# Performance work log

Measured on AMD Instinct MI355X. Metric: run time of the kernel, lower is better.

## Reference

```python
import jax, jax.numpy as jnp
import numpy as np
from functools import partial

NUM_HEADS = 8
EPS = 1e-12  # torch F.normalize default eps


def conv1x1(x, w):
    # x: [b,i,h,w], w: [o,i] -> [b,o,h,w]
    return jnp.einsum('oi,bihw->bohw', w, x)


def dwconv3x3(x, w):
    # depthwise 3x3, SAME padding; x: [b,c,h,w], w: [c,1,3,3]
    c = x.shape[1]
    return jax.lax.conv_general_dilated(
        x, w, window_strides=(1, 1), padding='SAME',
        dimension_numbers=('NCHW', 'OIHW', 'NCHW'), feature_group_count=c)


def setup_inputs() -> dict:
    key = jax.random.key(0)
    ks = jax.random.split(key, 16)
    b, dim, h, w = 2, 128, 256, 256
    d8 = dim // 8
    f = lambda k, shape, fan: (jax.random.normal(k, shape, jnp.float32) * (1.0 / np.sqrt(fan)))
    return {
        'x': jax.random.normal(ks[0], (b, dim, h, w), jnp.float32),
        'y': jax.random.normal(ks[1], (b, dim, h, w), jnp.float32),
        'qkv_w': f(ks[2], (dim * 3, dim), dim),
        'qkv_dw_w': f(ks[3], (dim * 3, 1, 3, 3), 9),
        'proj_w': f(ks[4], (dim, dim), dim),
        'sa_w1': f(ks[5], (d8, dim), dim),
        'sa_w2': f(ks[6], (d8, d8), d8),
        'sa_w3': f(ks[7], (1, d8), d8),
        'sp_w1': f(ks[8], (d8, dim), dim),
        'sp_w2': f(ks[9], (d8, d8), d8),
        'sp_w3': f(ks[10], (dim, d8), d8),
        'dw_w': f(ks[11], (dim, 1, 3, 3), 9),
        'temperature': jnp.ones((NUM_HEADS, 1, 1), jnp.float32),
    }


def reference(x, y, qkv_w, qkv_dw_w, proj_w, sa_w1, sa_w2, sa_w3,
              sp_w1, sp_w2, sp_w3, dw_w, temperature):
    b, c, h, w = x.shape
    hd = NUM_HEADS
    # QKV: 1x1 conv then depthwise 3x3
    qkv = dwconv3x3(conv1x1(x, qkv_w), qkv_dw_w)
    q, k, v = jnp.split(qkv, 3, axis=1)
    # Spatial attention gate from y: [b,1,h,w]
    sa = jax.nn.sigmoid(conv1x1(jax.nn.relu(conv1x1(jax.nn.relu(conv1x1(y, sa_w1)), sa_w2)), sa_w3))
    q = q * sa
    # b (head c) h w -> b head c (h w)
    shp = (b, hd, c // hd, h * w)
    q = q.reshape(shp)
    k = k.reshape(shp)
    v = v.reshape(shp)
    # L2 normalize along spatial axis (torch F.normalize semantics)
    q = q / jnp.maximum(jnp.linalg.norm(q, axis=-1, keepdims=True), EPS)
    k = k / jnp.maximum(jnp.linalg.norm(k, axis=-1, keepdims=True), EPS)
    # channel-wise attention: [b,head,c/head,c/head]
    attn = jnp.einsum('bhcn,bhdn->bhcd', q, k) * temperature
    attn = jax.nn.softmax(attn, axis=-1)
    out = jnp.einsum('bhcd,bhdn->bhcn', attn, v).reshape(b, c, h, w)
    # Spectral attention gate from out: [b,c]
    pooled = jnp.mean(out, axis=(2, 3))
    g = jax.nn.gelu(pooled @ sp_w1.T, approximate=False)
    g = jax.nn.gelu(g @ sp_w2.T, approximate=False)
    spec = jax.nn.sigmoid(g @ sp_w3.T)[:, :, None, None]
    y2 = dwconv3x3(y, dw_w) * spec
    return conv1x1(out + y2, proj_w)
```

## Files before the change

### kernel.cpp

```cpp
#include <hip/hip_runtime.h>
#include <hip/hip_bf16.h>

typedef __hip_bfloat16 bf16;
typedef __attribute__((ext_vector_type(8))) short short8;
typedef __attribute__((ext_vector_type(4))) int   int4v;
typedef __attribute__((ext_vector_type(4))) float float4v;

#define B_   2
#define C_   128
#define H_   256
#define W_   256
#define HW_  65536
#define HD_  8
#define CH_  16
#define C3_  384

static __device__ __forceinline__ float b2f(bf16 v) { return __bfloat162float(v); }
static __device__ __forceinline__ bf16  f2b(float v) { return __float2bfloat16(v); }
static __device__ __forceinline__ short b2s(bf16 v) { return *reinterpret_cast<short*>(&v); }
static __device__ __forceinline__ float su2f(short s) {
  return __uint_as_float(((unsigned)(unsigned short)s) << 16);
}
static __device__ __forceinline__ short8 smask(short8 v, int m) {
  int4v iv = *(int4v*)&v;
  iv = iv & m;
  return *(short8*)&iv;
}

__global__ void k_wprep(const float* __restrict__ qkv_w, const float* __restrict__ proj_w,
                        const float* __restrict__ sa_w1,
                        float* __restrict__ wt_qkvT, float* __restrict__ wt_proj,
                        float* __restrict__ wt_sa1, bf16* __restrict__ wt_qkv_bf,
                        bf16* __restrict__ wt_proj_bf, int do_bf) {
  int idx = blockIdx.x * 256 + threadIdx.x;
  if (idx < C3_ * C_) { int o = idx / C_, i = idx % C_; wt_qkvT[i * C3_ + o] = qkv_w[idx]; }
  if (idx < C_ * C_)  { int o = idx / C_, i = idx % C_; wt_proj[i * C_ + o] = proj_w[idx]; }
  if (idx < 16 * C_)  { int j = idx / C_, i = idx % C_; wt_sa1[i * 16 + j] = sa_w1[idx]; }
  if (do_bf && idx < C3_ * C_) {
    int o = idx / C_, k = idx % C_;
    int sk = ((((k >> 3) ^ (o & 7)) << 3) | (k & 7));
    wt_qkv_bf[o * C_ + sk] = f2b(qkv_w[idx]);
  }
  if (do_bf && idx < C_ * C_) {
    int o = idx / C_, k = idx % C_;
    int sk = ((((k >> 3) ^ (o & 7)) << 3) | (k & 7));
    wt_proj_bf[o * C_ + sk] = f2b(proj_w[idx]);
  }
}

__global__ void __launch_bounds__(256) k_sa(
    const float* __restrict__ y, const float* __restrict__ wt_sa1,
    const float* __restrict__ sa_w2, const float* __restrict__ sa_w3,
    float* __restrict__ sa) {
  int b = blockIdx.y;
  int p0 = (blockIdx.x * 256 + threadIdx.x) * 2;
  const float* yp = y + (size_t)b * C_ * HW_ + p0;
  float t1a[16], t1b[16];
#pragma unroll
  for (int j = 0; j < 16; ++j) { t1a[j] = 0.f; t1b[j] = 0.f; }
  for (int i = 0; i < C_; ++i) {
    float2 v = *(const float2*)(yp + (size_t)i * HW_);
    const float* wr = wt_sa1 + i * 16;
#pragma unroll
    for (int j = 0; j < 16; ++j) { t1a[j] = fmaf(wr[j], v.x, t1a[j]); t1b[j] = fmaf(wr[j], v.y, t1b[j]); }
  }
#pragma unroll
  for (int j = 0; j < 16; ++j) { t1a[j] = fmaxf(t1a[j], 0.f); t1b[j] = fmaxf(t1b[j], 0.f); }
  float t2a[16], t2b[16];
#pragma unroll
  for (int j = 0; j < 16; ++j) {
    float sx = 0.f, sy = 0.f;
#pragma unroll
    for (int l = 0; l < 16; ++l) { float w = sa_w2[j * 16 + l]; sx = fmaf(w, t1a[l], sx); sy = fmaf(w, t1b[l], sy); }
    t2a[j] = fmaxf(sx, 0.f); t2b[j] = fmaxf(sy, 0.f);
  }
  float sa3 = 0.f, sb3 = 0.f;
#pragma unroll
  for (int j = 0; j < 16; ++j) { float w = sa_w3[j]; sa3 = fmaf(w, t2a[j], sa3); sb3 = fmaf(w, t2b[j], sb3); }
  sa[(size_t)b * HW_ + p0]     = 1.f / (1.f + expf(-sa3));
  sa[(size_t)b * HW_ + p0 + 1] = 1.f / (1.f + expf(-sb3));
}

__global__ void __launch_bounds__(256) k_convm(
    const float* __restrict__ x, const bf16* __restrict__ wbf, bf16* __restrict__ pre) {
  __shared__ bf16 XT[2][64][128];
  __shared__ bf16 AT[128][128];
  int b = blockIdx.y;
  int p0 = blockIdx.x * 64;
  int t = threadIdx.x;

  {
    int p  = t & 63;
    int c0 = t >> 6;
    const float* xp = x + (size_t)b * C_ * HW_ + p0 + p;
#pragma unroll
    for (int it = 0; it < 4; ++it) {
      int c = c0 + it * 4;
      short8 hv, lv;
#pragma unroll
      for (int j = 0; j < 8; ++j) {
        float v = xp[(size_t)(c * 8 + j) * HW_];
        bf16 h = f2b(v);
        bf16 l = f2b(v - b2f(h));
        hv[j] = b2s(h); lv[j] = b2s(l);
      }
      int sc = c ^ (p & 7);
      *(short8*)&XT[0][p][sc * 8] = hv;
      *(short8*)&XT[1][p][sc * 8] = lv;
    }
  }

  int lane = t & 63, wave = t >> 6;
  int m = lane & 15, quad = lane >> 4;
  int wr = wave >> 1, wc = wave & 1;
  float4v acc[4][2];

  for (int mb = 0; mb < 3; ++mb) {
    __syncthreads();
    {
      const short8* src = (const short8*)(wbf + mb * C_ * C_);
      short8* dst = (short8*)&AT[0][0];
#pragma unroll
      for (int j = 0; j < 8; ++j)
        dst[j * 256 + t] = src[j * 256 + t];
    }
    __syncthreads();

#pragma unroll
    for (int mt = 0; mt < 4; ++mt)
#pragma unroll
      for (int nt = 0; nt < 2; ++nt)
#pragma unroll
        for (int e = 0; e < 4; ++e) acc[mt][nt][e] = 0.f;

#pragma unroll
    for (int kk = 0; kk < 4; ++kk) {
      int cidx = (((kk * 4 + quad) ^ (m & 7)) << 3);
      short8 af[4], bh[2], bl[2];
#pragma unroll
      for (int mt = 0; mt < 4; ++mt)
        af[mt] = *(const short8*)&AT[wr * 64 + mt * 16 + m][cidx];
#pragma unroll
      for (int nt = 0; nt < 2; ++nt) {
        bh[nt] = *(const short8*)&XT[0][wc * 32 + nt * 16 + m][cidx];
        bl[nt] = *(const short8*)&XT[1][wc * 32 + nt * 16 + m][cidx];
      }
#pragma unroll
      for (int mt = 0; mt < 4; ++mt)
#pragma unroll
        for (int nt = 0; nt < 2; ++nt) {
          acc[mt][nt] = __builtin_amdgcn_mfma_f32_16x16x32_bf16(af[mt], bh[nt], acc[mt][nt], 0, 0, 0);
          acc[mt][nt] = __builtin_amdgcn_mfma_f32_16x16x32_bf16(af[mt], bl[nt], acc[mt][nt], 0, 0, 0);
        }
    }

    bf16* op = pre + (size_t)b * C3_ * HW_ + (size_t)(mb * C_) * HW_ + p0;
#pragma unroll
    for (int mt = 0; mt < 4; ++mt)
#pragma unroll
      for (int nt = 0; nt < 2; ++nt)
#pragma unroll
        for (int reg = 0; reg < 4; ++reg) {
          int o = wr * 64 + mt * 16 + quad * 4 + reg;
          int p = wc * 32 + nt * 16 + m;
          op[(size_t)o * HW_ + p] = f2b(acc[mt][nt][reg]);
        }
  }
}

__global__ void __launch_bounds__(256) k_dwgram(
    const bf16* __restrict__ pre, const float* __restrict__ dww,
    const float* __restrict__ sa, float* __restrict__ attn_raw,
    float* __restrict__ ssq_q, float* __restrict__ ssq_k) {
  __shared__ char smem[65536];
  bf16 (*ring)[4][256][8] = (bf16 (*)[4][256][8])smem;
  bf16 (*dwb)[256] = (bf16 (*)[256])(smem + 49152);
  float* red = (float*)smem;

  int b = blockIdx.z, head = blockIdx.y, r0 = blockIdx.x * 8;
  int t = threadIdx.x;
  const bf16* preb = pre + (size_t)b * C3_ * HW_;
  const float* saw = sa + (size_t)b * HW_;

  auto loadrow = [&](int r) {
    int slot = (r + 3) % 3;
#pragma unroll
    for (int cg = 0; cg < 4; ++cg) {
      short8 hv;
      if (r < 0 || r >= H_) {
#pragma unroll
        for (int j = 0; j < 8; ++j) hv[j] = 0;
      } else {
#pragma unroll
        for (int j = 0; j < 8; ++j) {
          int c = cg * 8 + j;
          int och = (c < 16) ? (head * CH_ + c) : (C_ + head * CH_ + c - 16);
          hv[j] = b2s(preb[(size_t)och * HW_ + r * W_ + t]);
        }
      }
      *(short8*)&ring[slot][cg][t][0] = hv;
    }
  };
  loadrow(r0 - 1); loadrow(r0); loadrow(r0 + 1);
  __syncthreads();

  int lane = t & 63, wave = t >> 6;
  int m = lane & 15, quad = lane >> 4;
  int sch = t >> 3;
  int ccl = (t > 0) ? (t - 1) : 0;
  int ccr = (t < W_ - 1) ? (t + 1) : (W_ - 1);
  int mskl = (t > 0) ? -1 : 0;
  int mskr = (t < W_ - 1) ? -1 : 0;
  float4v acc = {0.f, 0.f, 0.f, 0.f};
  float sacc = 0.f;

  for (int rr = r0; rr < r0 + 8; ++rr) {
    float gate = saw[rr * W_ + t];
    float a[32];
#pragma unroll
    for (int c = 0; c < 32; ++c) a[c] = 0.f;
#pragma unroll
    for (int dy = -1; dy <= 1; ++dy) {
      int s = (rr + dy + 3) % 3;
#pragma unroll
      for (int cg = 0; cg < 4; ++cg) {
        const bf16* base = &ring[s][cg][0][0];
        short8 vl = smask(*(const short8*)(base + ccl * 8), mskl);
        short8 vc = *(const short8*)(base + (size_t)t * 8);
        short8 vr = smask(*(const short8*)(base + ccr * 8), mskr);
#pragma unroll
        for (int j = 0; j < 8; ++j) {
          int c = cg * 8 + j;
          int och = (c < 16) ? (head * CH_ + c) : (C_ + head * CH_ + c - 16);
          const float* wp = dww + och * 9 + (dy + 1) * 3;
          a[c] = fmaf(wp[0], su2f(vl[j]), a[c]);
          a[c] = fmaf(wp[1], su2f(vc[j]), a[c]);
          a[c] = fmaf(wp[2], su2f(vr[j]), a[c]);
        }
      }
    }
#pragma unroll
    for (int c = 0; c < 16; ++c) a[c] *= gate;
#pragma unroll
    for (int c = 0; c < 32; ++c) dwb[c][t ^ ((c & 7) << 3)] = f2b(a[c]);
    __syncthreads();
#pragma unroll
    for (int cn = 0; cn < 2; ++cn) {
      int p0 = wave * 64 + cn * 32;
      int ca = ((((p0 >> 3) + quad) ^ (m & 7)) << 3);
      short8 af = *(const short8*)&dwb[m][ca];
      short8 bfv = *(const short8*)&dwb[16 + m][ca];
      acc = __builtin_amdgcn_mfma_f32_16x16x32_bf16(af, bfv, acc, 0, 0, 0);
    }
#pragma unroll
    for (int it = 0; it < 4; ++it) {
      int c = (t & 7) + it * 8;
      int cs = c ^ (sch & 7);
      short8 v = *(const short8*)&dwb[sch][cs * 8];
#pragma unroll
      for (int j = 0; j < 8; ++j) { float f = su2f(v[j]); sacc = fmaf(f, f, sacc); }
    }
    if (rr < r0 + 7) loadrow(rr + 2);
    __syncthreads();
  }
  float* ar = attn_raw + ((size_t)b * HD_ + head) * 256;
#pragma unroll
  for (int reg = 0; reg < 4; ++reg)
    atomicAdd(&ar[(quad * 4 + reg) * 16 + m], acc[reg]);
  red[t] = sacc;
  __syncthreads();
  if (t < 32) {
    float s = 0.f;
#pragma unroll
    for (int k = 0; k < 8; ++k) s += red[t * 8 + k];
    if (t < 16) atomicAdd(&ssq_q[((size_t)b * HD_ + head) * CH_ + t], s);
    else        atomicAdd(&ssq_k[((size_t)b * HD_ + head) * CH_ + t - 16], s);
  }
}

__global__ void k_softmax(const float* __restrict__ attn_raw, const float* __restrict__ ssq_q,
                          const float* __restrict__ ssq_k, const float* __restrict__ temperature,
                          float* __restrict__ attn) {
  int row = threadIdx.x;
  int bh = row >> 4;
  int head = bh & 7;
  float temp = temperature[head];
  float nq = fmaxf(sqrtf(ssq_q[row]), 1e-12f);
  float v[16];
#pragma unroll
  for (int d = 0; d < 16; ++d) {
    float nk = fmaxf(sqrtf(ssq_k[bh * 16 + d]), 1e-12f);
    v[d] = attn_raw[row * 16 + d] / (nq * nk) * temp;
  }
  float m = -1e30f;
#pragma unroll
  for (int d = 0; d < 16; ++d) m = fmaxf(m, v[d]);
  float s = 0.f;
#pragma unroll
  for (int d = 0; d < 16; ++d) { v[d] = expf(v[d] - m); s += v[d]; }
  float inv = 1.f / s;
#pragma unroll
  for (int d = 0; d < 16; ++d) attn[row * 16 + d] = v[d] * inv;
}

__global__ void __launch_bounds__(256) k_out(
    const bf16* __restrict__ pre, const float* __restrict__ dww,
    const float* __restrict__ attn, float* __restrict__ outb) {
  __shared__ bf16 ring[3][2][256][8];
  int b = blockIdx.z, head = blockIdx.y, r0 = blockIdx.x * 8;
  int t = threadIdx.x;
  const bf16* preb = pre + (size_t)b * C3_ * HW_ + (size_t)(2 * C_ + head * CH_) * HW_;

  auto loadrow = [&](int r) {
    int slot = (r + 3) % 3;
#pragma unroll
    for (int cg = 0; cg < 2; ++cg) {
      short8 hv;
      if (r < 0 || r >= H_) {
#pragma unroll
        for (int j = 0; j < 8; ++j) hv[j] = 0;
      } else {
#pragma unroll
        for (int j = 0; j < 8; ++j)
          hv[j] = b2s(preb[(size_t)(cg * 8 + j) * HW_ + r * W_ + t]);
      }
      *(short8*)&ring[slot][cg][t][0] = hv;
    }
  };
  loadrow(r0 - 1); loadrow(r0); loadrow(r0 + 1);
  __syncthreads();
  const float* ap = attn + ((size_t)b * HD_ + head) * 256;
  int ccl = (t > 0) ? (t - 1) : 0;
  int ccr = (t < W_ - 1) ? (t + 1) : (W_ - 1);
  int mskl = (t > 0) ? -1 : 0;
  int mskr = (t < W_ - 1) ? -1 : 0;
  for (int rr = r0; rr < r0 + 8; ++rr) {
    float vv[16];
#pragma unroll
    for (int c = 0; c < 16; ++c) vv[c] = 0.f;
#pragma unroll
    for (int dy = -1; dy <= 1; ++dy) {
      int s = (rr + dy + 3) % 3;
#pragma unroll
      for (int cg = 0; cg < 2; ++cg) {
        const bf16* base = &ring[s][cg][0][0];
        short8 vl = smask(*(const short8*)(base + ccl * 8), mskl);
        short8 vc = *(const short8*)(base + (size_t)t * 8);
        short8 vr = smask(*(const short8*)(base + ccr * 8), mskr);
#pragma unroll
        for (int j = 0; j < 8; ++j) {
          int c = cg * 8 + j;
          const float* wp = dww + (2 * C_ + head * CH_ + c) * 9 + (dy + 1) * 3;
          vv[c] = fmaf(wp[0], su2f(vl[j]), vv[c]);
          vv[c] = fmaf(wp[1], su2f(vc[j]), vv[c]);
          vv[c] = fmaf(wp[2], su2f(vr[j]), vv[c]);
        }
      }
    }
    float* op = outb + ((size_t)b * C_ + head * CH_) * (size_t)HW_ + rr * W_ + t;
#pragma unroll
    for (int c2 = 0; c2 < 16; ++c2) {
      float s2 = 0.f;
#pragma unroll
      for (int d = 0; d < 16; ++d) s2 = fmaf(ap[c2 * 16 + d], vv[d], s2);
      op[(size_t)c2 * HW_] = s2;
    }
    __syncthreads();
    if (rr < r0 + 7) loadrow(rr + 2);
    __syncthreads();
  }
}

__global__ void k_pool(const float* __restrict__ outb, float* __restrict__ pooled) {
  int ch = blockIdx.x, b = blockIdx.y;
  const float* p = outb + ((size_t)b * C_ + ch) * (size_t)HW_;
  float s = 0.f;
  for (int i = threadIdx.x * 4; i < HW_; i += 1024) {
    float4 v = *(const float4*)(p + i);
    s += v.x + v.y + v.z + v.w;
  }
#pragma unroll
  for (int off = 32; off > 0; off >>= 1) s += __shfl_down(s, off);
  __shared__ float wsum[4];
  int lane = threadIdx.x & 63, wv = threadIdx.x >> 6;
  if (lane == 0) wsum[wv] = s;
  __syncthreads();
  if (threadIdx.x == 0) {
    float tt = wsum[0] + wsum[1] + wsum[2] + wsum[3];
    pooled[b * C_ + ch] = tt * (1.f / HW_);
  }
}

__global__ void k_spec(const float* __restrict__ pooled, const float* __restrict__ sp_w1,
                       const float* __restrict__ sp_w2, const float* __restrict__ sp_w3,
                       float* __restrict__ spec) {
  __shared__ float g1[2][16], g2[2][16];
  int tid = threadIdx.x;
  const float RS2 = 0.70710678118654752f;
  if (tid < 32) {
    int b = tid >> 4, j = tid & 15;
    float s = 0.f;
    for (int i = 0; i < C_; ++i) s = fmaf(sp_w1[j * C_ + i], pooled[b * C_ + i], s);
    g1[b][j] = 0.5f * s * (1.f + erff(s * RS2));
  }
  __syncthreads();
  if (tid < 32) {
    int b = tid >> 4, j = tid & 15;
    float s = 0.f;
    for (int l = 0; l < 16; ++l) s = fmaf(sp_w2[j * 16 + l], g1[b][l], s);
    g2[b][j] = 0.5f * s * (1.f + erff(s * RS2));
  }
  __syncthreads();
  {
    int b = tid >> 7, o = tid & 127;
    float s = 0.f;
    for (int jj = 0; jj < 16; ++jj) s = fmaf(sp_w3[o * 16 + jj], g2[b][jj], s);
    spec[b * C_ + o] = 1.f / (1.f + expf(-s));
  }
}

__global__ void __launch_bounds__(256) k_z(
    const float* __restrict__ y, const float* __restrict__ dww,
    const float* __restrict__ spec, float* __restrict__ dout) {
  int b = blockIdx.z, ch = blockIdx.y;
  int row = blockIdx.x * 4 + (threadIdx.x >> 6);
  int c0 = (threadIdx.x & 63) * 4;
  const float* yb = y + ((size_t)b * C_ + ch) * HW_;
  const float* wp = dww + ch * 9;
  float acc[4] = {0.f, 0.f, 0.f, 0.f};
#pragma unroll
  for (int dy = -1; dy <= 1; ++dy) {
    int rrow = row + dy;
    if (rrow < 0 || rrow >= H_) continue;
    const float* yr = yb + rrow * W_;
    float4 cv = *(const float4*)(yr + c0);
    float lf = (c0 > 0) ? yr[c0 - 1] : 0.f;
    float rt = (c0 + 4 < W_) ? yr[c0 + 4] : 0.f;
    float w0 = wp[(dy + 1) * 3], w1 = wp[(dy + 1) * 3 + 1], w2 = wp[(dy + 1) * 3 + 2];
    float v[6] = {lf, cv.x, cv.y, cv.z, cv.w, rt};
#pragma unroll
    for (int j = 0; j < 4; ++j)
      acc[j] = fmaf(w0, v[j], fmaf(w1, v[j + 1], fmaf(w2, v[j + 2], acc[j])));
  }
  float sp = spec[b * C_ + ch];
  float* dp = dout + ((size_t)b * C_ + ch) * HW_ + row * W_ + c0;
  float4 ov = *(const float4*)dp;
  ov.x += acc[0] * sp; ov.y += acc[1] * sp; ov.z += acc[2] * sp; ov.w += acc[3] * sp;
  *(float4*)dp = ov;
}

__global__ void __launch_bounds__(256) k_projm(
    const bf16* __restrict__ wpb, float* __restrict__ dout) {
  __shared__ bf16 XT[2][64][128];
  __shared__ bf16 AT[128][128];
  int b = blockIdx.y;
  int p0 = blockIdx.x * 64;
  int t = threadIdx.x;

  {
    const short8* src = (const short8*)wpb;
    short8* dst = (short8*)&AT[0][0];
#pragma unroll
    for (int j = 0; j < 8; ++j)
      dst[j * 256 + t] = src[j * 256 + t];
  }
  {
    int p  = t & 63;
    int c0 = t >> 6;
    const float* xp = dout + (size_t)b * C_ * HW_ + p0 + p;
#pragma unroll
    for (int it = 0; it < 4; ++it) {
      int c = c0 + it * 4;
      short8 hv, lv;
#pragma unroll
      for (int j = 0; j < 8; ++j) {
        float v = xp[(size_t)(c * 8 + j) * HW_];
        bf16 h = f2b(v);
        bf16 l = f2b(v - b2f(h));
        hv[j] = b2s(h); lv[j] = b2s(l);
      }
      int sc = c ^ (p & 7);
      *(short8*)&XT[0][p][sc * 8] = hv;
      *(short8*)&XT[1][p][sc * 8] = lv;
    }
  }
  __syncthreads();

  int lane = t & 63, wave = t >> 6;
  int m = lane & 15, quad = lane >> 4;
  int wr = wave >> 1, wc = wave & 1;
  float4v acc[4][2];
#pragma unroll
  for (int mt = 0; mt < 4; ++mt)
#pragma unroll
    for (int nt = 0; nt < 2; ++nt)
#pragma unroll
      for (int e = 0; e < 4; ++e) acc[mt][nt][e] = 0.f;

#pragma unroll
  for (int kk = 0; kk < 4; ++kk) {
    int cidx = (((kk * 4 + quad) ^ (m & 7)) << 3);
    short8 af[4], bh[2], bl[2];
#pragma unroll
    for (int mt = 0; mt < 4; ++mt)
      af[mt] = *(const short8*)&AT[wr * 64 + mt * 16 + m][cidx];
#pragma unroll
    for (int nt = 0; nt < 2; ++nt) {
      bh[nt] = *(const short8*)&XT[0][wc * 32 + nt * 16 + m][cidx];
      bl[nt] = *(const short8*)&XT[1][wc * 32 + nt * 16 + m][cidx];
    }
#pragma unroll
    for (int mt = 0; mt < 4; ++mt)
#pragma unroll
      for (int nt = 0; nt < 2; ++nt) {
        acc[mt][nt] = __builtin_amdgcn_mfma_f32_16x16x32_bf16(af[mt], bh[nt], acc[mt][nt], 0, 0, 0);
        acc[mt][nt] = __builtin_amdgcn_mfma_f32_16x16x32_bf16(af[mt], bl[nt], acc[mt][nt], 0, 0, 0);
      }
  }

  float* op = dout + (size_t)b * C_ * HW_ + p0;
#pragma unroll
  for (int mt = 0; mt < 4; ++mt)
#pragma unroll
    for (int nt = 0; nt < 2; ++nt)
#pragma unroll
      for (int reg = 0; reg < 4; ++reg) {
        int o = wr * 64 + mt * 16 + quad * 4 + reg;
        int p = wc * 32 + nt * 16 + m;
        op[(size_t)o * HW_ + p] = acc[mt][nt][reg];
      }
}

__global__ void __launch_bounds__(256) k_gram_fb(
    const float* __restrict__ x, const float* __restrict__ wt_qkvT,
    const float* __restrict__ dww, const float* __restrict__ sa,
    float* __restrict__ attn_raw, float* __restrict__ ssq_q, float* __restrict__ ssq_k) {
  __shared__ bf16 ring[3][32][256];
  __shared__ bf16 dwb[32][256];
  int b = blockIdx.z, head = blockIdx.y, r0 = blockIdx.x * 8;
  int t = threadIdx.x;
  const float* xb = x + (size_t)b * C_ * HW_;
  const float* saw = sa + (size_t)b * HW_;
  auto convrow = [&](int r) {
    int slot = (r + 3) % 3;
    if (r < 0 || r >= H_) {
#pragma unroll
      for (int c = 0; c < 32; ++c) ring[slot][c][t] = f2b(0.f);
      return;
    }
    float acc[32];
#pragma unroll
    for (int c = 0; c < 32; ++c) acc[c] = 0.f;
    const float* xp = xb + r * W_ + t;
    const float* wq = wt_qkvT + head * CH_;
    const float* wk = wt_qkvT + C_ + head * CH_;
    for (int i = 0; i < C_; ++i) {
      float xv = xp[(size_t)i * HW_];
      const float* w1 = wq + i * C3_;
      const float* w2 = wk + i * C3_;
#pragma unroll
      for (int c = 0; c < 16; ++c) acc[c]      = fmaf(w1[c], xv, acc[c]);
#pragma unroll
      for (int c = 0; c < 16; ++c) acc[16 + c] = fmaf(w2[c], xv, acc[16 + c]);
    }
#pragma unroll
    for (int c = 0; c < 32; ++c) ring[slot][c][t] = f2b(acc[c]);
  };
  convrow(r0 - 1); convrow(r0); convrow(r0 + 1);
  __syncthreads();
  int c = t >> 4, d = t & 15;
  float gacc = 0.f, sacc = 0.f;
  for (int rr = r0; rr < r0 + 8; ++rr) {
    float gate = saw[rr * W_ + t];
    for (int ch = 0; ch < 32; ++ch) {
      int och = (ch < 16) ? (head * CH_ + ch) : (C_ + head * CH_ + ch - 16);
      float a = 0.f;
#pragma unroll
      for (int dy = -1; dy <= 1; ++dy) {
        int s = (rr + dy + 3) % 3;
#pragma unroll
        for (int dx = -1; dx <= 1; ++dx) {
          int cc = t + dx;
          if (cc < 0 || cc >= W_) continue;
          a = fmaf(dww[och * 9 + (dy + 1) * 3 + dx + 1], b2f(ring[s][ch][cc]), a);
        }
      }
      if (ch < 16) a *= gate;
      dwb[ch][t] = f2b(a);
    }
    __syncthreads();
    for (int p = 0; p < 256; ++p) {
      int pp = (p + 4 * d + 2 * c) & 255;
      gacc = fmaf(b2f(dwb[c][pp]), b2f(dwb[16 + d][pp]), gacc);
    }
    if (t < 32) {
      for (int p = 0; p < 256; ++p) {
        int pp = (p + 2 * t) & 255;
        float v = b2f(dwb[t][pp]);
        sacc = fmaf(v, v, sacc);
      }
    }
    if (rr < r0 + 7) convrow(rr + 2);
    __syncthreads();
  }
  atomicAdd(&attn_raw[(((size_t)b * HD_ + head) * CH_ + c) * CH_ + d], gacc);
  if (t < 16)      atomicAdd(&ssq_q[((size_t)b * HD_ + head) * CH_ + t], sacc);
  else if (t < 32) atomicAdd(&ssq_k[((size_t)b * HD_ + head) * CH_ + t - 16], sacc);
}

__global__ void __launch_bounds__(256) k_out_fb(
    const float* __restrict__ x, const float* __restrict__ wt_qkvT,
    const float* __restrict__ dww, const float* __restrict__ attn,
    float* __restrict__ outb) {
  __shared__ bf16 ring[3][16][256];
  int b = blockIdx.z, head = blockIdx.y, r0 = blockIdx.x * 8;
  int t = threadIdx.x;
  const float* xb = x + (size_t)b * C_ * HW_;
  auto convrow = [&](int r) {
    int slot = (r + 3) % 3;
    if (r < 0 || r >= H_) {
#pragma unroll
      for (int c = 0; c < 16; ++c) ring[slot][c][t] = f2b(0.f);
      return;
    }
    float acc[16];
#pragma unroll
    for (int c = 0; c < 16; ++c) acc[c] = 0.f;
    const float* xp = xb + r * W_ + t;
    const float* wv = wt_qkvT + 2 * C_ + head * CH_;
    for (int i = 0; i < C_; ++i) {
      float xv = xp[(size_t)i * HW_];
      const float* w1 = wv + i * C3_;
#pragma unroll
      for (int c = 0; c < 16; ++c) acc[c] = fmaf(w1[c], xv, acc[c]);
    }
#pragma unroll
    for (int c = 0; c < 16; ++c) ring[slot][c][t] = f2b(acc[c]);
  };
  convrow(r0 - 1); convrow(r0); convrow(r0 + 1);
  __syncthreads();
  const float* ap = attn + ((size_t)b * HD_ + head) * 256;
  for (int rr = r0; rr < r0 + 8; ++rr) {
    float vv[16];
#pragma unroll
    for (int ch = 0; ch < 16; ++ch) {
      int och = 2 * C_ + head * CH_ + ch;
      float a = 0.f;
#pragma unroll
      for (int dy = -1; dy <= 1; ++dy) {
        int s = (rr + dy + 3) % 3;
#pragma unroll
        for (int dx = -1; dx <= 1; ++dx) {
          int cc = t + dx;
          if (cc < 0 || cc >= W_) continue;
          a = fmaf(dww[och * 9 + (dy + 1) * 3 + dx + 1], b2f(ring[s][ch][cc]), a);
        }
      }
      vv[ch] = a;
    }
    float* op = outb + ((size_t)b * C_ + head * CH_) * (size_t)HW_ + rr * W_ + t;
#pragma unroll
    for (int c2 = 0; c2 < 16; ++c2) {
      float s = 0.f;
#pragma unroll
      for (int d = 0; d < 16; ++d) s = fmaf(ap[c2 * 16 + d], vv[d], s);
      op[(size_t)c2 * HW_] = s;
    }
    __syncthreads();
    if (rr < r0 + 7) convrow(rr + 2);
    __syncthreads();
  }
}

__global__ void __launch_bounds__(256) k_zproj_fb(
    const float* __restrict__ y, const float* __restrict__ dwwz,
    const float* __restrict__ spec, const float* __restrict__ wt_proj,
    float* __restrict__ dout) {
  __shared__ bf16 zt[128][256];
  int b = blockIdx.y, r = blockIdx.x;
  int t = threadIdx.x;
  const float* yb = y + (size_t)b * C_ * HW_;
  float* db = dout + (size_t)b * C_ * HW_;
  for (int ch = 0; ch < C_; ++ch) {
    float a = 0.f;
#pragma unroll
    for (int dy = -1; dy <= 1; ++dy) {
      int hh = r + dy;
      if (hh < 0 || hh >= H_) continue;
      const float* row = yb + (size_t)ch * HW_ + hh * W_;
#pragma unroll
      for (int dx = -1; dx <= 1; ++dx) {
        int cc = t + dx;
        if (cc < 0 || cc >= W_) continue;
        a = fmaf(dwwz[ch * 9 + (dy + 1) * 3 + dx + 1], row[cc], a);
      }
    }
    float z = db[(size_t)ch * HW_ + r * W_ + t] + a * spec[b * C_ + ch];
    zt[ch][t] = f2b(z);
  }
  __syncthreads();
#pragma unroll
  for (int half = 0; half < 2; ++half) {
    float acc[64];
#pragma unroll
    for (int o = 0; o < 64; ++o) acc[o] = 0.f;
    for (int i = 0; i < C_; ++i) {
      float zv = b2f(zt[i][t]);
      const float* wr = wt_proj + i * C_ + half * 64;
#pragma unroll
      for (int o = 0; o < 64; ++o) acc[o] = fmaf(wr[o], zv, acc[o]);
    }
#pragma unroll
    for (int o = 0; o < 64; ++o)
      db[(size_t)(half * 64 + o) * HW_ + r * W_ + t] = acc[o];
  }
}

extern "C" void kernel_launch(void* const* d_in, const int* in_sizes, int n_in,
                              void* d_out, int out_size, void* d_ws, size_t ws_size,
                              hipStream_t stream) {
  const float* x        = (const float*)d_in[0];
  const float* y        = (const float*)d_in[1];
  const float* qkv_w    = (const float*)d_in[2];
  const float* qkv_dw_w = (const float*)d_in[3];
  const float* proj_w   = (const float*)d_in[4];
  const float* sa_w1    = (const float*)d_in[5];
  const float* sa_w2    = (const float*)d_in[6];
  const float* sa_w3    = (const float*)d_in[7];
  const float* sp_w1    = (const float*)d_in[8];
  const float* sp_w2    = (const float*)d_in[9];
  const float* sp_w3    = (const float*)d_in[10];
  const float* dw_w     = (const float*)d_in[11];
  const float* temp     = (const float*)d_in[12];
  float* out = (float*)d_out;

  char* ws = (char*)d_ws;
  float* attn_raw = (float*)(ws + 0);
  float* ssq_q    = (float*)(ws + 16384);
  float* ssq_k    = (float*)(ws + 17408);
  float* attn     = (float*)(ws + 18432);
  float* pooled   = (float*)(ws + 34816);
  float* spec     = (float*)(ws + 35840);
  float* wt_qkvT  = (float*)(ws + 36864);
  float* wt_proj  = (float*)(ws + 233472);
  float* wt_sa1   = (float*)(ws + 299008);
  float* sa       = (float*)(ws + 307200);
  bf16*  wt_qkv_bf = (bf16*)(ws + 835584);
  bf16*  wt_proj_bf= (bf16*)(ws + 933888);
  bf16*  pre      = (bf16*) (ws + 1048576);
  const size_t NEED = 1048576 + 100663296;
  bool big = ws_size >= NEED;

  hipMemsetAsync(ws, 0, 18432, stream);

  k_wprep<<<192, 256, 0, stream>>>(qkv_w, proj_w, sa_w1, wt_qkvT, wt_proj, wt_sa1,
                                   wt_qkv_bf, wt_proj_bf, big ? 1 : 0);
  k_sa<<<dim3(HW_ / 512, B_), 256, 0, stream>>>(y, wt_sa1, sa_w2, sa_w3, sa);
  if (big) {
    k_convm<<<dim3(HW_ / 64, B_), 256, 0, stream>>>(x, wt_qkv_bf, pre);
    k_dwgram<<<dim3(H_ / 8, HD_, B_), 256, 0, stream>>>(pre, qkv_dw_w, sa,
                                                        attn_raw, ssq_q, ssq_k);
    k_softmax<<<1, 256, 0, stream>>>(attn_raw, ssq_q, ssq_k, temp, attn);
    k_out<<<dim3(H_ / 8, HD_, B_), 256, 0, stream>>>(pre, qkv_dw_w, attn, out);
  } else {
    k_gram_fb<<<dim3(H_ / 8, HD_, B_), 256, 0, stream>>>(x, wt_qkvT, qkv_dw_w, sa,
                                                         attn_raw, ssq_q, ssq_k);
    k_softmax<<<1, 256, 0, stream>>>(attn_raw, ssq_q, ssq_k, temp, attn);
    k_out_fb<<<dim3(H_ / 8, HD_, B_), 256, 0, stream>>>(x, wt_qkvT, qkv_dw_w, attn, out);
  }
  k_pool<<<dim3(C_, B_), 256, 0, stream>>>(out, pooled);
  k_spec<<<1, 256, 0, stream>>>(pooled, sp_w1, sp_w2, sp_w3, spec);
  if (big) {
    k_z<<<dim3(H_ / 4, C_, B_), 256, 0, stream>>>(y, dw_w, spec, out);
    k_projm<<<dim3(HW_ / 64, B_), 256, 0, stream>>>(wt_proj_bf, out);
  } else {
    k_zproj_fb<<<dim3(H_, B_), 256, 0, stream>>>(y, dw_w, spec, wt_proj, out);
  }
}
```

Baseline: 451.2 us.

## Fuse pooling into k_out, prefetch rows into registers, move ssq into registers

```diff
diff --git a/kernel.cpp b/kernel.cpp
--- a/kernel.cpp
+++ b/kernel.cpp
@@ -168,71 +168,80 @@
   }
 }
 
-__global__ void __launch_bounds__(256) k_dwgram(
+__global__ void __launch_bounds__(256, 2) k_dwgram(
     const bf16* __restrict__ pre, const float* __restrict__ dww,
     const float* __restrict__ sa, float* __restrict__ attn_raw,
     float* __restrict__ ssq_q, float* __restrict__ ssq_k) {
   __shared__ char smem[65536];
-  bf16 (*ring)[4][256][8] = (bf16 (*)[4][256][8])smem;
   bf16 (*dwb)[256] = (bf16 (*)[256])(smem + 49152);
-  float* red = (float*)smem;
 
   int b = blockIdx.z, head = blockIdx.y, r0 = blockIdx.x * 8;
   int t = threadIdx.x;
   const bf16* preb = pre + (size_t)b * C3_ * HW_;
   const float* saw = sa + (size_t)b * HW_;
 
-  auto loadrow = [&](int r) {
-    int slot = (r + 3) % 3;
+  auto fetchrow = [&](int r, short8 pf[4]) {
 #pragma unroll
     for (int cg = 0; cg < 4; ++cg) {
-      short8 hv;
-      if (r < 0 || r >= H_) {
-#pragma unroll
-        for (int j = 0; j < 8; ++j) hv[j] = 0;
-      } else {
+#pragma unroll
+      for (int j = 0; j < 8; ++j) {
+        int c = cg * 8 + j;
+        int och = (c < 16) ? (head * CH_ + c) : (C_ + head * CH_ + c - 16);
+        pf[cg][j] = (r < 0 || r >= H_) ? (short)0
+                    : b2s(preb[(size_t)och * HW_ + r * W_ + t]);
+      }
+    }
+  };
+  auto writerow = [&](int soff, const short8 pf[4]) {
+#pragma unroll
+    for (int cg = 0; cg < 4; ++cg)
+      *(short8*)(smem + soff + cg * 4096 + t * 16) = pf[cg];
+  };
+
+  {
+    short8 pf0[4], pf1[4], pf2[4];
+    fetchrow(r0 - 1, pf0); fetchrow(r0, pf1); fetchrow(r0 + 1, pf2);
+    writerow(0, pf0); writerow(16384, pf1); writerow(32768, pf2);
+  }
+  __syncthreads();
+
+  int lane = t & 63, wave = t >> 6;
+  int m = lane & 15, quad = lane >> 4;
+  int colL = ((t > 0) ? (t - 1) : 0) * 16;
+  int colC = t * 16;
+  int colR = ((t < W_ - 1) ? (t + 1) : (W_ - 1)) * 16;
+  int mskl = (t > 0) ? -1 : 0;
+  int mskr = (t < W_ - 1) ? -1 : 0;
+  float4v acc = {0.f, 0.f, 0.f, 0.f};
+  float ssq[32];
+#pragma unroll
+  for (int c = 0; c < 32; ++c) ssq[c] = 0.f;
+
+  int so0 = 0, so1 = 16384, so2 = 32768;
+
+  for (int i = 0; i < 8; ++i) {
+    int rr = r0 + i;
+    short8 pfn[4];
+    if (i < 7) fetchrow(rr + 2, pfn);
+    float gate = saw[rr * W_ + t];
+
+    float a[32];
+#pragma unroll
+    for (int c = 0; c < 32; ++c) a[c] = 0.f;
+#pragma unroll
+    for (int dy = 0; dy < 3; ++dy) {
+      int soff = (dy == 0) ? so0 : ((dy == 1) ? so1 : so2);
+#pragma unroll
+      for (int cg = 0; cg < 4; ++cg) {
+        const char* base = smem + soff + cg * 4096;
+        short8 vl = smask(*(const short8*)(base + colL), mskl);
+        short8 vc = *(const short8*)(base + colC);
+        short8 vr = smask(*(const short8*)(base + colR), mskr);
 #pragma unroll
         for (int j = 0; j < 8; ++j) {
           int c = cg * 8 + j;
           int och = (c < 16) ? (head * CH_ + c) : (C_ + head * CH_ + c - 16);
-          hv[j] = b2s(preb[(size_t)och * HW_ + r * W_ + t]);
-        }
-      }
-      *(short8*)&ring[slot][cg][t][0] = hv;
-    }
-  };
-  loadrow(r0 - 1); loadrow(r0); loadrow(r0 + 1);
-  __syncthreads();
-
-  int lane = t & 63, wave = t >> 6;
-  int m = lane & 15, quad = lane >> 4;
-  int sch = t >> 3;
-  int ccl = (t > 0) ? (t - 1) : 0;
-  int ccr = (t < W_ - 1) ? (t + 1) : (W_ - 1);
-  int mskl = (t > 0) ? -1 : 0;
-  int mskr = (t < W_ - 1) ? -1 : 0;
-  float4v acc = {0.f, 0.f, 0.f, 0.f};
-  float sacc = 0.f;
-
-  for (int rr = r0; rr < r0 + 8; ++rr) {
-    float gate = saw[rr * W_ + t];
-    float a[32];
-#pragma unroll
-    for (int c = 0; c < 32; ++c) a[c] = 0.f;
-#pragma unroll
-    for (int dy = -1; dy <= 1; ++dy) {
-      int s = (rr + dy + 3) % 3;
-#pragma unroll
-      for (int cg = 0; cg < 4; ++cg) {
-        const bf16* base = &ring[s][cg][0][0];
-        short8 vl = smask(*(const short8*)(base + ccl * 8), mskl);
-        short8 vc = *(const short8*)(base + (size_t)t * 8);
-        short8 vr = smask(*(const short8*)(base + ccr * 8), mskr);
-#pragma unroll
-        for (int j = 0; j < 8; ++j) {
-          int c = cg * 8 + j;
-          int och = (c < 16) ? (head * CH_ + c) : (C_ + head * CH_ + c - 16);
-          const float* wp = dww + och * 9 + (dy + 1) * 3;
+          const float* wp = dww + och * 9 + dy * 3;
           a[c] = fmaf(wp[0], su2f(vl[j]), a[c]);
           a[c] = fmaf(wp[1], su2f(vc[j]), a[c]);
           a[c] = fmaf(wp[2], su2f(vr[j]), a[c]);
@@ -241,6 +250,8 @@
     }
 #pragma unroll
     for (int c = 0; c < 16; ++c) a[c] *= gate;
+#pragma unroll
+    for (int c = 0; c < 32; ++c) ssq[c] = fmaf(a[c], a[c], ssq[c]);
 #pragma unroll
     for (int c = 0; c < 32; ++c) dwb[c][t ^ ((c & 7) << 3)] = f2b(a[c]);
     __syncthreads();
@@ -252,29 +263,29 @@
       short8 bfv = *(const short8*)&dwb[16 + m][ca];
       acc = __builtin_amdgcn_mfma_f32_16x16x32_bf16(af, bfv, acc, 0, 0, 0);
     }
-#pragma unroll
-    for (int it = 0; it < 4; ++it) {
-      int c = (t & 7) + it * 8;
-      int cs = c ^ (sch & 7);
-      short8 v = *(const short8*)&dwb[sch][cs * 8];
-#pragma unroll
-      for (int j = 0; j < 8; ++j) { float f = su2f(v[j]); sacc = fmaf(f, f, sacc); }
-    }
-    if (rr < r0 + 7) loadrow(rr + 2);
-    __syncthreads();
-  }
+    if (i < 7) writerow(so0, pfn);
+    __syncthreads();
+    int tmp = so0; so0 = so1; so1 = so2; so2 = tmp;
+  }
+
   float* ar = attn_raw + ((size_t)b * HD_ + head) * 256;
 #pragma unroll
   for (int reg = 0; reg < 4; ++reg)
     atomicAdd(&ar[(quad * 4 + reg) * 16 + m], acc[reg]);
-  red[t] = sacc;
-  __syncthreads();
-  if (t < 32) {
-    float s = 0.f;
-#pragma unroll
-    for (int k = 0; k < 8; ++k) s += red[t * 8 + k];
-    if (t < 16) atomicAdd(&ssq_q[((size_t)b * HD_ + head) * CH_ + t], s);
-    else        atomicAdd(&ssq_k[((size_t)b * HD_ + head) * CH_ + t - 16], s);
+
+#pragma unroll
+  for (int c = 0; c < 32; ++c) {
+#pragma unroll
+    for (int off = 32; off > 0; off >>= 1)
+      ssq[c] += __shfl_xor(ssq[c], off, 64);
+  }
+  if (lane == 0) {
+    float* sq = ssq_q + ((size_t)b * HD_ + head) * CH_;
+    float* sk = ssq_k + ((size_t)b * HD_ + head) * CH_;
+#pragma unroll
+    for (int c = 0; c < 16; ++c) atomicAdd(&sq[c], ssq[c]);
+#pragma unroll
+    for (int c = 16; c < 32; ++c) atomicAdd(&sk[c - 16], ssq[c]);
   }
 }
 
@@ -303,54 +314,70 @@
   for (int d = 0; d < 16; ++d) attn[row * 16 + d] = v[d] * inv;
 }
 
-__global__ void __launch_bounds__(256) k_out(
+__global__ void __launch_bounds__(256, 4) k_out(
     const bf16* __restrict__ pre, const float* __restrict__ dww,
-    const float* __restrict__ attn, float* __restrict__ outb) {
-  __shared__ bf16 ring[3][2][256][8];
+    const float* __restrict__ attn, float* __restrict__ outb,
+    float* __restrict__ pooled) {
+  __shared__ char smem[24576];
   int b = blockIdx.z, head = blockIdx.y, r0 = blockIdx.x * 8;
   int t = threadIdx.x;
   const bf16* preb = pre + (size_t)b * C3_ * HW_ + (size_t)(2 * C_ + head * CH_) * HW_;
 
-  auto loadrow = [&](int r) {
-    int slot = (r + 3) % 3;
+  auto fetchrow = [&](int r, short8 pf[2]) {
 #pragma unroll
     for (int cg = 0; cg < 2; ++cg) {
-      short8 hv;
-      if (r < 0 || r >= H_) {
-#pragma unroll
-        for (int j = 0; j < 8; ++j) hv[j] = 0;
-      } else {
-#pragma unroll
-        for (int j = 0; j < 8; ++j)
-          hv[j] = b2s(preb[(size_t)(cg * 8 + j) * HW_ + r * W_ + t]);
-      }
-      *(short8*)&ring[slot][cg][t][0] = hv;
+#pragma unroll
+      for (int j = 0; j < 8; ++j)
+        pf[cg][j] = (r < 0 || r >= H_) ? (short)0
+                    : b2s(preb[(size_t)(cg * 8 + j) * HW_ + r * W_ + t]);
     }
   };
-  loadrow(r0 - 1); loadrow(r0); loadrow(r0 + 1);
+  auto writerow = [&](int soff, const short8 pf[2]) {
+#pragma unroll
+    for (int cg = 0; cg < 2; ++cg)
+      *(short8*)(smem + soff + cg * 4096 + t * 16) = pf[cg];
+  };
+
+  {
+    short8 pf0[2], pf1[2], pf2[2];
+    fetchrow(r0 - 1, pf0); fetchrow(r0, pf1); fetchrow(r0 + 1, pf2);
+    writerow(0, pf0); writerow(8192, pf1); writerow(16384, pf2);
+  }
   __syncthreads();
+
   const float* ap = attn + ((size_t)b * HD_ + head) * 256;
-  int ccl = (t > 0) ? (t - 1) : 0;
-  int ccr = (t < W_ - 1) ? (t + 1) : (W_ - 1);
+  int colL = ((t > 0) ? (t - 1) : 0) * 16;
+  int colC = t * 16;
+  int colR = ((t < W_ - 1) ? (t + 1) : (W_ - 1)) * 16;
   int mskl = (t > 0) ? -1 : 0;
   int mskr = (t < W_ - 1) ? -1 : 0;
-  for (int rr = r0; rr < r0 + 8; ++rr) {
+  float psum[16];
+#pragma unroll
+  for (int c = 0; c < 16; ++c) psum[c] = 0.f;
+
+  int so0 = 0, so1 = 8192, so2 = 16384;
+
+  for (int i = 0; i < 8; ++i) {
+    int rr = r0 + i;
+    short8 pfn[2];
+    if (i < 7) fetchrow(rr + 2, pfn);
+
     float vv[16];
 #pragma unroll
     for (int c = 0; c < 16; ++c) vv[c] = 0.f;
 #pragma unroll
-    for (int dy = -1; dy <= 1; ++dy) {
-      int s = (rr + dy + 3) % 3;
+    for (int dy = 0; dy < 3; ++dy) {
+      int soff = (dy == 0) ? so0 : ((dy == 1) ? so1 : so2);
 #pragma unroll
       for (int cg = 0; cg < 2; ++cg) {
-        const bf16* base = &ring[s][cg][0][0];
-        short8 vl = smask(*(const short8*)(base + ccl * 8), mskl);
-        short8 vc = *(const short8*)(base + (size_t)t * 8);
-        short8 vr = smask(*(const short8*)(base + ccr * 8), mskr);
+        const char* base = smem + soff + cg * 4096;
+        short8 vl = smask(*(const short8*)(base + colL), mskl);
+        short8 vc = *(const short8*)(base + colC);
+        short8 vr = smask(*(const short8*)(base + colR), mskr);
 #pragma unroll
         for (int j = 0; j < 8; ++j) {
           int c = cg * 8 + j;
-          const float* wp = dww + (2 * C_ + head * CH_ + c) * 9 + (dy + 1) * 3;
+          const float* wp = dww + (2 * C_ + head * CH_ + c) * 9 + dy * 3;
           vv[c] = fmaf(wp[0], su2f(vl[j]), vv[c]);
           vv[c] = fmaf(wp[1], su2f(vc[j]), vv[c]);
           vv[c] = fmaf(wp[2], su2f(vr[j]), vv[c]);
@@ -364,10 +391,25 @@
 #pragma unroll
       for (int d = 0; d < 16; ++d) s2 = fmaf(ap[c2 * 16 + d], vv[d], s2);
       op[(size_t)c2 * HW_] = s2;
-    }
-    __syncthreads();
-    if (rr < r0 + 7) loadrow(rr + 2);
-    __syncthreads();
+      psum[c2] += s2;
+    }
+    __syncthreads();
+    if (i < 7) writerow(so0, pfn);
+    __syncthreads();
+    int tmp = so0; so0 = so1; so1 = so2; so2 = tmp;
+  }
+
+  int lane = t & 63;
+#pragma unroll
+  for (int c = 0; c < 16; ++c) {
+#pragma unroll
+    for (int off = 32; off > 0; off >>= 1)
+      psum[c] += __shfl_xor(psum[c], off, 64);
+  }
+  if (lane == 0) {
+    float* pp = pooled + (size_t)b * C_ + head * CH_;
+#pragma unroll
+    for (int c = 0; c < 16; ++c) atomicAdd(&pp[c], psum[c]);
   }
 }
 
@@ -393,14 +435,14 @@
 
 __global__ void k_spec(const float* __restrict__ pooled, const float* __restrict__ sp_w1,
                        const float* __restrict__ sp_w2, const float* __restrict__ sp_w3,
-                       float* __restrict__ spec) {
+                       float* __restrict__ spec, float pscale) {
   __shared__ float g1[2][16], g2[2][16];
   int tid = threadIdx.x;
   const float RS2 = 0.70710678118654752f;
   if (tid < 32) {
     int b = tid >> 4, j = tid & 15;
     float s = 0.f;
-    for (int i = 0; i < C_; ++i) s = fmaf(sp_w1[j * C_ + i], pooled[b * C_ + i], s);
+    for (int i = 0; i < C_; ++i) s = fmaf(sp_w1[j * C_ + i], pooled[b * C_ + i] * pscale, s);
     g1[b][j] = 0.5f * s * (1.f + erff(s * RS2));
   }
   __syncthreads();
@@ -752,6 +794,7 @@
   bool big = ws_size >= NEED;
 
   hipMemsetAsync(ws, 0, 18432, stream);
+  hipMemsetAsync(pooled, 0, 1024, stream);
 
   k_wprep<<<192, 256, 0, stream>>>(qkv_w, proj_w, sa_w1, wt_qkvT, wt_proj, wt_sa1,
                                    wt_qkv_bf, wt_proj_bf, big ? 1 : 0);
@@ -761,19 +804,17 @@
     k_dwgram<<<dim3(H_ / 8, HD_, B_), 256, 0, stream>>>(pre, qkv_dw_w, sa,
                                                         attn_raw, ssq_q, ssq_k);
     k_softmax<<<1, 256, 0, stream>>>(attn_raw, ssq_q, ssq_k, temp, attn);
-    k_out<<<dim3(H_ / 8, HD_, B_), 256, 0, stream>>>(pre, qkv_dw_w, attn, out);
+    k_out<<<dim3(H_ / 8, HD_, B_), 256, 0, stream>>>(pre, qkv_dw_w, attn, out, pooled);
+    k_spec<<<1, 256, 0, stream>>>(pooled, sp_w1, sp_w2, sp_w3, spec, 1.f / HW_);
+    k_z<<<dim3(H_ / 4, C_, B_), 256, 0, stream>>>(y, dw_w, spec, out);
+    k_projm<<<dim3(HW_ / 64, B_), 256, 0, stream>>>(wt_proj_bf, out);
   } else {
     k_gram_fb<<<dim3(H_ / 8, HD_, B_), 256, 0, stream>>>(x, wt_qkvT, qkv_dw_w, sa,
                                                          attn_raw, ssq_q, ssq_k);
     k_softmax<<<1, 256, 0, stream>>>(attn_raw, ssq_q, ssq_k, temp, attn);
     k_out_fb<<<dim3(H_ / 8, HD_, B_), 256, 0, stream>>>(x, wt_qkvT, qkv_dw_w, attn, out);
-  }
-  k_pool<<<dim3(C_, B_), 256, 0, stream>>>(out, pooled);
-  k_spec<<<1, 256, 0, stream>>>(pooled, sp_w1, sp_w2, sp_w3, spec);
-  if (big) {
-    k_z<<<dim3(H_ / 4, C_, B_), 256, 0, stream>>>(y, dw_w, spec, out);
-    k_projm<<<dim3(HW_ / 64, B_), 256, 0, stream>>>(wt_proj_bf, out);
-  } else {
+    k_pool<<<dim3(C_, B_), 256, 0, stream>>>(out, pooled);
+    k_spec<<<1, 256, 0, stream>>>(pooled, sp_w1, sp_w2, sp_w3, spec, 1.f);
     k_zproj_fb<<<dim3(H_, B_), 256, 0, stream>>>(y, dw_w, spec, wt_proj, out);
   }
 }
```

Result: slower. 720.4 us (+59.7%).
